# Optimization experiments

Measured on AMD Instinct MI355X. Metric: run time of the kernel, lower is better.

## Reference

```python
import jax, jax.numpy as jnp
import numpy as np

B, D, L = 2, 1024, 4096   # batch, channels (= num_heads), seq len
FS = 4                    # filter_size
DEPTH = 11                # ceil(log2((L-1)/(FS-1)+1))
LN_EPS = 1e-5


def setup_inputs() -> dict:
    key = jax.random.key(0)
    ks = jax.random.split(key, 7)
    return {
        "x": jax.random.normal(ks[0], (B, D, L), jnp.float32),
        "h0": jax.random.normal(ks[1], (D, 1, FS), jnp.float32) * 0.2,
        "h1": jax.random.normal(ks[2], (D, 1, FS), jnp.float32) * 0.2,
        "w_mix": jax.random.normal(ks[3], (D, D), jnp.float32) / np.sqrt(D),
        "b_mix": jnp.zeros((D,), jnp.float32),
        "ln_gamma": jnp.ones((D,), jnp.float32),
        "ln_beta": jnp.zeros((D,), jnp.float32),
    }


def _dw_conv(a, h, dilation):
    # depthwise (groups = D) dilated conv1d, cross-correlation like torch
    return jax.lax.conv_general_dilated(
        a, h, window_strides=(1,), padding='VALID',
        rhs_dilation=(dilation,),
        dimension_numbers=('NCH', 'OIH', 'NCH'),
        feature_group_count=D)


def reference(x, h0, h1, w_mix, b_mix, ln_gamma, ln_beta):
    # --- multires conv tree ---
    a = x
    dilation = 1
    a_list, b_list = [], []
    for _ in range(DEPTH):
        pad = dilation * (FS - 1)
        ap = jnp.pad(a, ((0, 0), (0, 0), (pad, 0)))  # left causal pad
        b = _dw_conv(ap, h1, dilation)
        a = _dw_conv(ap, h0, dilation)
        a_list.append(a)
        b_list.append(b)
        dilation *= 2
    # --- gated combination across scales (deepest level first) ---
    a_rev = a_list[::-1]
    b_rev = b_list[::-1]
    y = jnp.zeros_like(x)
    gated = None
    for i in range(DEPTH):
        if i + 1 < DEPTH:
            gated = jax.nn.sigmoid(a_rev[i]) * b_rev[i + 1]
        # last iteration reuses the previous gated tensor (matches original)
        y = y + gated
    # --- 1x1 channel mix (Dropout1d is identity in eval) + residual ---
    mixed = jnp.einsum('oc,bcl->bol', w_mix, y) + b_mix[None, :, None]
    z = mixed + x
    # --- LayerNorm over channel dim ---
    mu = jnp.mean(z, axis=1, keepdims=True)
    var = jnp.mean(jnp.square(z - mu), axis=1, keepdims=True)
    out = (z - mu) * jax.lax.rsqrt(var + LN_EPS)
    out = out * ln_gamma[None, :, None] + ln_beta[None, :, None]
    return out
```

## Files before the change

### kernel.cpp

```cpp
#include <hip/hip_runtime.h>
#include <hip/hip_bf16.h>

#define NB 2
#define ND 1024
#define NL 4096
#define NFS 4
#define NDEPTH 11
#define LN_EPS 1e-5f

#define BM 128
#define BN 128
#define BK 32
#define NKI (ND / BK)

#define CPAD 1536
#define CBUF (CPAD + NL)

typedef __bf16 bf16x8 __attribute__((ext_vector_type(8)));
typedef float f32x4 __attribute__((ext_vector_type(4)));

__device__ __forceinline__ unsigned short f2bf(float f) {
    __hip_bfloat16 h = __float2bfloat16(f);
    unsigned short u;
    __builtin_memcpy(&u, &h, 2);
    return u;
}

__device__ __forceinline__ float bf2f(unsigned short u) {
    unsigned int ui = (unsigned int)u << 16;
    float f;
    __builtin_memcpy(&f, &ui, 4);
    return f;
}

__device__ __forceinline__ unsigned int pack2bf(float lo, float hi) {
    return (unsigned int)f2bf(lo) | ((unsigned int)f2bf(hi) << 16);
}

__device__ __forceinline__ float sigm(float v) {
    return __builtin_amdgcn_rcpf(1.f + __expf(-v));
}

__device__ __forceinline__ void llds16(const void* g, void* l) {
    __builtin_amdgcn_global_load_lds(
        (const __attribute__((address_space(1))) unsigned int*)g,
        (__attribute__((address_space(3))) unsigned int*)l, 16, 0, 0);
}

__global__ __launch_bounds__(256) void wconv_kernel(const float* __restrict__ w,
                                                    unsigned short* __restrict__ wbf) {
    const int idx8 = (blockIdx.x * 256 + threadIdx.x) * 8;
    const float4 v0 = *reinterpret_cast<const float4*>(w + idx8);
    const float4 v1 = *reinterpret_cast<const float4*>(w + idx8 + 4);
    uint4 o;
    o.x = pack2bf(v0.x, v0.y);
    o.y = pack2bf(v0.z, v0.w);
    o.z = pack2bf(v1.x, v1.y);
    o.w = pack2bf(v1.z, v1.w);
    *reinterpret_cast<uint4*>(wbf + idx8) = o;
}

__global__ __launch_bounds__(256) void conv_cascade_kernel(const float* __restrict__ x,
                                                           const float* __restrict__ h0,
                                                           const float* __restrict__ h1,
                                                           unsigned short* __restrict__ ybf) {
    __shared__ float a_sh[2 * CBUF];
    const int row = blockIdx.x;
    const int d = row & (ND - 1);
    const int t = threadIdx.x;

#pragma unroll
    for (int j = 0; j < 2; ++j)
#pragma unroll
        for (int i = 0; i < CPAD / 256; ++i)
            a_sh[j * CBUF + i * 256 + t] = 0.f;

    const float* xrow = x + (size_t)row * NL;

    float h0c[NFS], h1c[NFS];
#pragma unroll
    for (int k = 0; k < NFS; ++k) {
        h0c[k] = h0[d * NFS + k];
        h1c[k] = h1[d * NFS + k];
    }

    float cur[4][4], yacc[4][4], bprev[4][4];
#pragma unroll
    for (int c = 0; c < 4; ++c) {
        const float4 v = *reinterpret_cast<const float4*>(xrow + c * 1024 + t * 4);
        cur[c][0] = v.x; cur[c][1] = v.y; cur[c][2] = v.z; cur[c][3] = v.w;
        *reinterpret_cast<float4*>(&a_sh[CPAD + c * 1024 + t * 4]) = v;
#pragma unroll
        for (int j = 0; j < 4; ++j) { yacc[c][j] = 0.f; bprev[c][j] = 0.f; }
    }
    __syncthreads();

    int rb = 0, wb = CBUF;

#define CONV_CHUNK(c, A1, A2, A3, SC, WB)                                            \
    {                                                                                \
        float an[4], bn[4];                                                          \
        _Pragma("unroll") for (int j = 0; j < 4; ++j) {                              \
            an[j] = h0c[3] * cur[c][j] + h0c[2] * (A1)[j] + h0c[1] * (A2)[j] +       \
                    h0c[0] * (A3)[j];                                                \
            bn[j] = h1c[3] * cur[c][j] + h1c[2] * (A1)[j] + h1c[1] * (A2)[j] +       \
                    h1c[0] * (A3)[j];                                                \
        }                                                                            \
        if (WB) {                                                                    \
            float4 wv; wv.x = an[0]; wv.y = an[1]; wv.z = an[2]; wv.w = an[3];       \
            *reinterpret_cast<float4*>(&a_sh[wb + CPAD + (c)*1024 + t * 4]) = wv;    \
        }                                                                            \
        if ((SC) > 0.f) {                                                            \
            _Pragma("unroll") for (int j = 0; j < 4; ++j)                            \
                yacc[c][j] += (SC)*sigm(an[j]) * bprev[c][j];                        \
        }                                                                            \
        _Pragma("unroll") for (int j = 0; j < 4; ++j) {                              \
            cur[c][j] = an[j];                                                       \
            bprev[c][j] = bn[j];                                                     \
        }                                                                            \
    }

#pragma unroll
    for (int c = 0; c < 4; ++c) {
        const int A = rb + CPAD + c * 1024 + t * 4;
        const float4 m1 = *reinterpret_cast<const float4*>(&a_sh[A - 4]);
        const float a1[4] = {m1.w, cur[c][0], cur[c][1], cur[c][2]};
        const float a2[4] = {m1.z, m1.w, cur[c][0], cur[c][1]};
        const float a3[4] = {m1.y, m1.z, m1.w, cur[c][0]};
        CONV_CHUNK(c, a1, a2, a3, 0.f, 1)
    }
    { const int tmp = rb; rb = wb; wb = tmp; }
    __syncthreads();

#pragma unroll
    for (int c = 0; c < 4; ++c) {
        const int A = rb + CPAD + c * 1024 + t * 4;
        const float4 m1 = *reinterpret_cast<const float4*>(&a_sh[A - 4]);
        const float4 m2 = *reinterpret_cast<const float4*>(&a_sh[A - 8]);
        const float a1[4] = {m1.z, m1.w, cur[c][0], cur[c][1]};
        const float a2[4] = {m1.x, m1.y, m1.z, m1.w};
        const float a3[4] = {m2.z, m2.w, m1.x, m1.y};
        CONV_CHUNK(c, a1, a2, a3, 2.f, 1)
    }
    { const int tmp = rb; rb = wb; wb = tmp; }
    __syncthreads();

    int dil = 4;
#pragma unroll 1
    for (int lev = 2; lev <= 8; ++lev) {
#pragma unroll
        for (int c = 0; c < 4; ++c) {
            const int A = rb + CPAD + c * 1024 + t * 4;
            const float4 b1 = *reinterpret_cast<const float4*>(&a_sh[A - dil]);
            const float4 b2 = *reinterpret_cast<const float4*>(&a_sh[A - 2 * dil]);
            const float4 b3 = *reinterpret_cast<const float4*>(&a_sh[A - 3 * dil]);
            const float a1[4] = {b1.x, b1.y, b1.z, b1.w};
            const float a2[4] = {b2.x, b2.y, b2.z, b2.w};
            const float a3[4] = {b3.x, b3.y, b3.z, b3.w};
            CONV_CHUNK(c, a1, a2, a3, 1.f, 1)
        }
        { const int tmp = rb; rb = wb; wb = tmp; }
        dil <<= 1;
        __syncthreads();
    }

#pragma unroll
    for (int c = 0; c < 4; ++c) {
        const int A = rb + CPAD + c * 1024 + t * 4;
        const float4 b1 = *reinterpret_cast<const float4*>(&a_sh[A - 512]);
        const float4 b2 = *reinterpret_cast<const float4*>(&a_sh[A - 1024]);
        const float4 b3 = *reinterpret_cast<const float4*>(&a_sh[A - 1536]);
        const float a1[4] = {b1.x, b1.y, b1.z, b1.w};
        const float a2[4] = {b2.x, b2.y, b2.z, b2.w};
        const float a3[4] = {b3.x, b3.y, b3.z, b3.w};
        CONV_CHUNK(c, a1, a2, a3, 1.f, 0)
    }

#pragma unroll
    for (int c = 0; c < 4; ++c) {
#pragma unroll
        for (int j = 0; j < 4; ++j) {
            const float a1 = (c >= 1) ? cur[c - 1][j] : 0.f;
            const float a2 = (c >= 2) ? cur[c - 2][j] : 0.f;
            const float a3 = (c >= 3) ? cur[c - 3][j] : 0.f;
            const float an = h0c[3] * cur[c][j] + h0c[2] * a1 + h0c[1] * a2 + h0c[0] * a3;
            yacc[c][j] += sigm(an) * bprev[c][j];
        }
    }
#undef CONV_CHUNK

#pragma unroll
    for (int c = 0; c < 4; ++c) {
        ushort4 o;
        o.x = f2bf(yacc[c][0]);
        o.y = f2bf(yacc[c][1]);
        o.z = f2bf(yacc[c][2]);
        o.w = f2bf(yacc[c][3]);
        *reinterpret_cast<ushort4*>(ybf + (size_t)row * NL + c * 1024 + t * 4) = o;
    }
}

__global__ __launch_bounds__(256) void transpose_kernel(const unsigned short* __restrict__ ybf,
                                                        unsigned short* __restrict__ yT) {
    __shared__ unsigned short tile[64][66];
    const int l0 = blockIdx.x * 64;
    const int c0 = blockIdx.y * 64;
    const int b = blockIdx.z;
    const int t = threadIdx.x;
    const int li = t & 63, cg = t >> 6;
#pragma unroll
    for (int k = 0; k < 16; ++k) {
        const int ci = cg * 16 + k;
        tile[ci][li] = ybf[(size_t)(b * ND + c0 + ci) * NL + l0 + li];
    }
    __syncthreads();
    const int ci2 = t & 63, lg = t >> 6;
#pragma unroll
    for (int k = 0; k < 16; ++k) {
        const int li2 = lg * 16 + k;
        yT[((size_t)b * NL + l0 + li2) * ND + c0 + ci2] = tile[ci2][li2];
    }
}

__global__ __launch_bounds__(256) void gemm_kernel(const unsigned short* __restrict__ wbf,
                                                   const unsigned short* __restrict__ yT,
                                                   const float* __restrict__ bmix,
                                                   unsigned short* __restrict__ mixed) {
    __shared__ unsigned short As[2][BM][BK];
    __shared__ unsigned short Bs[2][BN][BK];

    const int n0 = blockIdx.x * BN;
    const int m0 = blockIdx.y * BM;
    const int b = blockIdx.z;
    const int t = threadIdx.x;
    const int lane = t & 63, wid = t >> 6;
    const int wr = wid >> 1, wc = wid & 1;
    const int fr = lane & 15;
    const int fk = (lane >> 4) * 8;

    const int srow = wid * 32 + (lane >> 2);
    const int sk = (lane & 3) * 8;
    const unsigned short* Ag = wbf + (size_t)(m0 + srow) * ND + sk;
    const unsigned short* Bg = yT + ((size_t)b * NL + n0 + srow) * ND + sk;
    unsigned short* AsD0[2] = {&As[0][wid * 32][0], &As[1][wid * 32][0]};
    unsigned short* AsD1[2] = {&As[0][wid * 32 + 16][0], &As[1][wid * 32 + 16][0]};
    unsigned short* BsD0[2] = {&Bs[0][wid * 32][0], &Bs[1][wid * 32][0]};
    unsigned short* BsD1[2] = {&Bs[0][wid * 32 + 16][0], &Bs[1][wid * 32 + 16][0]};

    f32x4 acc[4][4];
#pragma unroll
    for (int mi = 0; mi < 4; ++mi)
#pragma unroll
        for (int ni = 0; ni < 4; ++ni)
            acc[mi][ni] = (f32x4){0.f, 0.f, 0.f, 0.f};

    llds16(Ag, AsD0[0]);
    llds16(Ag + 16 * ND, AsD1[0]);
    llds16(Bg, BsD0[0]);
    llds16(Bg + 16 * ND, BsD1[0]);
    asm volatile("s_waitcnt vmcnt(0)" ::: "memory");
    __builtin_amdgcn_s_barrier();

    int cur = 0;
#pragma unroll 1
    for (int ki = 0; ki < NKI; ++ki) {
        if (ki + 1 < NKI) {
            const int kt = (ki + 1) * BK;
            llds16(Ag + kt, AsD0[cur ^ 1]);
            llds16(Ag + kt + 16 * ND, AsD1[cur ^ 1]);
            llds16(Bg + kt, BsD0[cur ^ 1]);
            llds16(Bg + kt + 16 * ND, BsD1[cur ^ 1]);
        }

        bf16x8 af[4], bv[4];
#pragma unroll
        for (int mi = 0; mi < 4; ++mi)
            af[mi] = *reinterpret_cast<const bf16x8*>(&As[cur][wr * 64 + mi * 16 + fr][fk]);
#pragma unroll
        for (int ni = 0; ni < 4; ++ni)
            bv[ni] = *reinterpret_cast<const bf16x8*>(&Bs[cur][wc * 64 + ni * 16 + fr][fk]);
#pragma unroll
        for (int mi = 0; mi < 4; ++mi)
#pragma unroll
            for (int ni = 0; ni < 4; ++ni)
                acc[mi][ni] = __builtin_amdgcn_mfma_f32_16x16x32_bf16(af[mi], bv[ni],
                                                                      acc[mi][ni], 0, 0, 0);

        asm volatile("s_waitcnt vmcnt(0)" ::: "memory");
        __builtin_amdgcn_s_barrier();
        cur ^= 1;
    }

    const size_t bbase = (size_t)b * ND * NL;
#pragma unroll
    for (int mi = 0; mi < 4; ++mi) {
#pragma unroll
        for (int r = 0; r < 4; ++r) {
            const int o = m0 + wr * 64 + mi * 16 + (lane >> 4) * 4 + r;
            const float bm = bmix[o];
            const size_t rowbase = bbase + (size_t)o * NL;
#pragma unroll
            for (int ni = 0; ni < 4; ++ni) {
                const int l = n0 + wc * 64 + ni * 16 + fr;
                mixed[rowbase + l] = f2bf(acc[mi][ni][r] + bm);
            }
        }
    }
}

__global__ __launch_bounds__(512) void ln_kernel(const unsigned short* __restrict__ mixed,
                                                 const float* __restrict__ x,
                                                 const float* __restrict__ gamma,
                                                 const float* __restrict__ beta,
                                                 float* __restrict__ out) {
    const int b = blockIdx.y;
    const int l0 = blockIdx.x * 32;
    const int tl = threadIdx.x & 31, tg = threadIdx.x >> 5;
    const size_t base = (size_t)b * ND * NL + l0 + tl;

    float zv[64];
    float s = 0.f, q = 0.f;
#pragma unroll
    for (int j = 0; j < 64; ++j) {
        const size_t idx = base + (size_t)(tg + j * 16) * NL;
        const float v = bf2f(mixed[idx]) + x[idx];
        zv[j] = v;
        s += v;
        q += v * v;
    }

    __shared__ float sred[16][33], qred[16][33];
    __shared__ float mu_s[32], rs_s[32];
    sred[tg][tl] = s;
    qred[tg][tl] = q;
    __syncthreads();
    if (tg == 0) {
        float S = 0.f, Q = 0.f;
#pragma unroll
        for (int g = 0; g < 16; ++g) {
            S += sred[g][tl];
            Q += qred[g][tl];
        }
        const float mu = S * (1.f / ND);
        const float var = Q * (1.f / ND) - mu * mu;
        mu_s[tl] = mu;
        rs_s[tl] = rsqrtf(var + LN_EPS);
    }
    __syncthreads();
    const float mu = mu_s[tl], rs = rs_s[tl];
#pragma unroll
    for (int j = 0; j < 64; ++j) {
        const int c = tg + j * 16;
        out[base + (size_t)c * NL] = (zv[j] - mu) * rs * gamma[c] + beta[c];
    }
}

extern "C" void kernel_launch(void* const* d_in, const int* in_sizes, int n_in,
                              void* d_out, int out_size, void* d_ws, size_t ws_size,
                              hipStream_t stream) {
    (void)in_sizes; (void)n_in; (void)out_size; (void)ws_size;
    const float* x = (const float*)d_in[0];
    const float* h0 = (const float*)d_in[1];
    const float* h1 = (const float*)d_in[2];
    const float* wmix = (const float*)d_in[3];
    const float* bmix = (const float*)d_in[4];
    const float* gamma = (const float*)d_in[5];
    const float* beta = (const float*)d_in[6];
    float* out = (float*)d_out;

    char* ws = (char*)d_ws;
    unsigned short* ybf = (unsigned short*)(ws);
    unsigned short* yT = (unsigned short*)(ws + (size_t)16 * 1024 * 1024);
    unsigned short* wbf = (unsigned short*)(ws + (size_t)32 * 1024 * 1024);
    unsigned short* mixed = (unsigned short*)(ws + (size_t)34 * 1024 * 1024);

    wconv_kernel<<<dim3(ND * ND / (256 * 8)), 256, 0, stream>>>(wmix, wbf);
    conv_cascade_kernel<<<dim3(NB * ND), 256, 0, stream>>>(x, h0, h1, ybf);
    transpose_kernel<<<dim3(NL / 64, ND / 64, NB), 256, 0, stream>>>(ybf, yT);
    gemm_kernel<<<dim3(NL / BN, ND / BM, NB), 256, 0, stream>>>(wbf, yT, bmix, mixed);
    ln_kernel<<<dim3(NL / 32, NB), 512, 0, stream>>>(mixed, x, gamma, beta, out);
}
```

Baseline: 105.8 us.

## Single-buffer conv cascade with 512 threads; triple-buffer GEMM LDS pipeline

The conv cascade kernel now runs 512 threads per row, each handling two 4-wide chunks. It uses a single LDS buffer with a larger causal pad instead of ping-pong buffers, and an extra barrier separates the reads from the writes. Levels 9 and 10 move into the shared-memory loop and the final level reads from LDS. The GEMM switches from double to triple buffering with two stages prefetched ahead and a partial vmcnt wait, so global loads overlap more MFMA work. This adds barriers in the conv kernel and more LDS use in the GEMM, which may lower occupancy.

```diff
diff --git a/kernel.cpp b/kernel.cpp
--- a/kernel.cpp
+++ b/kernel.cpp
@@ -12,8 +12,9 @@
 #define BN 128
 #define BK 32
 #define NKI (ND / BK)
-
-#define CPAD 1536
+#define ASZ (BM * BK)
+
+#define CPAD 3072
 #define CBUF (CPAD + NL)
 
 typedef __bf16 bf16x8 __attribute__((ext_vector_type(8)));
@@ -60,20 +61,17 @@
     *reinterpret_cast<uint4*>(wbf + idx8) = o;
 }
 
-__global__ __launch_bounds__(256) void conv_cascade_kernel(const float* __restrict__ x,
-                                                           const float* __restrict__ h0,
-                                                           const float* __restrict__ h1,
-                                                           unsigned short* __restrict__ ybf) {
-    __shared__ float a_sh[2 * CBUF];
+__global__ __launch_bounds__(512, 8) void conv_cascade_kernel(const float* __restrict__ x,
+                                                              const float* __restrict__ h0,
+                                                              const float* __restrict__ h1,
+                                                              unsigned short* __restrict__ ybf) {
+    __shared__ float a_sh[CBUF];
     const int row = blockIdx.x;
     const int d = row & (ND - 1);
     const int t = threadIdx.x;
 
 #pragma unroll
-    for (int j = 0; j < 2; ++j)
-#pragma unroll
-        for (int i = 0; i < CPAD / 256; ++i)
-            a_sh[j * CBUF + i * 256 + t] = 0.f;
+    for (int i = 0; i < CPAD / 512; ++i) a_sh[i * 512 + t] = 0.f;
 
     const float* xrow = x + (size_t)row * NL;
 
@@ -84,32 +82,28 @@
         h1c[k] = h1[d * NFS + k];
     }
 
-    float cur[4][4], yacc[4][4], bprev[4][4];
-#pragma unroll
-    for (int c = 0; c < 4; ++c) {
-        const float4 v = *reinterpret_cast<const float4*>(xrow + c * 1024 + t * 4);
+    float cur[2][4], yacc[2][4], bprev[2][4];
+#pragma unroll
+    for (int c = 0; c < 2; ++c) {
+        const float4 v = *reinterpret_cast<const float4*>(xrow + c * 2048 + t * 4);
         cur[c][0] = v.x; cur[c][1] = v.y; cur[c][2] = v.z; cur[c][3] = v.w;
-        *reinterpret_cast<float4*>(&a_sh[CPAD + c * 1024 + t * 4]) = v;
+        *reinterpret_cast<float4*>(&a_sh[CPAD + c * 2048 + t * 4]) = v;
 #pragma unroll
         for (int j = 0; j < 4; ++j) { yacc[c][j] = 0.f; bprev[c][j] = 0.f; }
     }
     __syncthreads();
 
-    int rb = 0, wb = CBUF;
-
-#define CONV_CHUNK(c, A1, A2, A3, SC, WB)                                            \
+#define CONV_MATH(c, A1, A2, A3, an, bn)                                             \
+    _Pragma("unroll") for (int j = 0; j < 4; ++j) {                                  \
+        an[j] = h0c[3] * cur[c][j] + h0c[2] * (A1)[j] + h0c[1] * (A2)[j] +           \
+                h0c[0] * (A3)[j];                                                    \
+        bn[j] = h1c[3] * cur[c][j] + h1c[2] * (A1)[j] + h1c[1] * (A2)[j] +           \
+                h1c[0] * (A3)[j];                                                    \
+    }
+#define CONV_FIN(c, an, bn, SC)                                                      \
     {                                                                                \
-        float an[4], bn[4];                                                          \
-        _Pragma("unroll") for (int j = 0; j < 4; ++j) {                              \
-            an[j] = h0c[3] * cur[c][j] + h0c[2] * (A1)[j] + h0c[1] * (A2)[j] +       \
-                    h0c[0] * (A3)[j];                                                \
-            bn[j] = h1c[3] * cur[c][j] + h1c[2] * (A1)[j] + h1c[1] * (A2)[j] +       \
-                    h1c[0] * (A3)[j];                                                \
-        }                                                                            \
-        if (WB) {                                                                    \
-            float4 wv; wv.x = an[0]; wv.y = an[1]; wv.z = an[2]; wv.w = an[3];       \
-            *reinterpret_cast<float4*>(&a_sh[wb + CPAD + (c)*1024 + t * 4]) = wv;    \
-        }                                                                            \
+        float4 wv; wv.x = an[0]; wv.y = an[1]; wv.z = an[2]; wv.w = an[3];           \
+        *reinterpret_cast<float4*>(&a_sh[CPAD + (c)*2048 + t * 4]) = wv;             \
         if ((SC) > 0.f) {                                                            \
             _Pragma("unroll") for (int j = 0; j < 4; ++j)                            \
                 yacc[c][j] += (SC)*sigm(an[j]) * bprev[c][j];                        \
@@ -120,83 +114,111 @@
         }                                                                            \
     }
 
-#pragma unroll
-    for (int c = 0; c < 4; ++c) {
-        const int A = rb + CPAD + c * 1024 + t * 4;
-        const float4 m1 = *reinterpret_cast<const float4*>(&a_sh[A - 4]);
-        const float a1[4] = {m1.w, cur[c][0], cur[c][1], cur[c][2]};
-        const float a2[4] = {m1.z, m1.w, cur[c][0], cur[c][1]};
-        const float a3[4] = {m1.y, m1.z, m1.w, cur[c][0]};
-        CONV_CHUNK(c, a1, a2, a3, 0.f, 1)
-    }
-    { const int tmp = rb; rb = wb; wb = tmp; }
-    __syncthreads();
-
-#pragma unroll
-    for (int c = 0; c < 4; ++c) {
-        const int A = rb + CPAD + c * 1024 + t * 4;
-        const float4 m1 = *reinterpret_cast<const float4*>(&a_sh[A - 4]);
-        const float4 m2 = *reinterpret_cast<const float4*>(&a_sh[A - 8]);
-        const float a1[4] = {m1.z, m1.w, cur[c][0], cur[c][1]};
-        const float a2[4] = {m1.x, m1.y, m1.z, m1.w};
-        const float a3[4] = {m2.z, m2.w, m1.x, m1.y};
-        CONV_CHUNK(c, a1, a2, a3, 2.f, 1)
-    }
-    { const int tmp = rb; rb = wb; wb = tmp; }
-    __syncthreads();
+    float an0[4], bn0[4], an1[4], bn1[4];
+
+    {
+        {
+            const int A = CPAD + 0 * 2048 + t * 4;
+            const float4 m1 = *reinterpret_cast<const float4*>(&a_sh[A - 4]);
+            const float a1[4] = {m1.w, cur[0][0], cur[0][1], cur[0][2]};
+            const float a2[4] = {m1.z, m1.w, cur[0][0], cur[0][1]};
+            const float a3[4] = {m1.y, m1.z, m1.w, cur[0][0]};
+            CONV_MATH(0, a1, a2, a3, an0, bn0)
+        }
+        {
+            const int A = CPAD + 1 * 2048 + t * 4;
+            const float4 m1 = *reinterpret_cast<const float4*>(&a_sh[A - 4]);
+            const float a1[4] = {m1.w, cur[1][0], cur[1][1], cur[1][2]};
+            const float a2[4] = {m1.z, m1.w, cur[1][0], cur[1][1]};
+            const float a3[4] = {m1.y, m1.z, m1.w, cur[1][0]};
+            CONV_MATH(1, a1, a2, a3, an1, bn1)
+        }
+        __syncthreads();
+        CONV_FIN(0, an0, bn0, 0.f)
+        CONV_FIN(1, an1, bn1, 0.f)
+        __syncthreads();
+    }
+
+    {
+        {
+            const int A = CPAD + 0 * 2048 + t * 4;
+            const float4 m1 = *reinterpret_cast<const float4*>(&a_sh[A - 4]);
+            const float4 m2 = *reinterpret_cast<const float4*>(&a_sh[A - 8]);
+            const float a1[4] = {m1.z, m1.w, cur[0][0], cur[0][1]};
+            const float a2[4] = {m1.x, m1.y, m1.z, m1.w};
+            const float a3[4] = {m2.z, m2.w, m1.x, m1.y};
+            CONV_MATH(0, a1, a2, a3, an0, bn0)
+        }
+        {
+            const int A = CPAD + 1 * 2048 + t * 4;
+            const float4 m1 = *reinterpret_cast<const float4*>(&a_sh[A - 4]);
+            const float4 m2 = *reinterpret_cast<const float4*>(&a_sh[A - 8]);
+            const float a1[4] = {m1.z, m1.w, cur[1][0], cur[1][1]};
+            const float a2[4] = {m1.x, m1.y, m1.z, m1.w};
+            const float a3[4] = {m2.z, m2.w, m1.x, m1.y};
+            CONV_MATH(1, a1, a2, a3, an1, bn1)
+        }
+        __syncthreads();
+        CONV_FIN(0, an0, bn0, 2.f)
+        CONV_FIN(1, an1, bn1, 2.f)
+        __syncthreads();
+    }
 
     int dil = 4;
 #pragma unroll 1
-    for (int lev = 2; lev <= 8; ++lev) {
-#pragma unroll
-        for (int c = 0; c < 4; ++c) {
-            const int A = rb + CPAD + c * 1024 + t * 4;
+    for (int lev = 2; lev <= 9; ++lev) {
+        {
+            const int A = CPAD + 0 * 2048 + t * 4;
             const float4 b1 = *reinterpret_cast<const float4*>(&a_sh[A - dil]);
             const float4 b2 = *reinterpret_cast<const float4*>(&a_sh[A - 2 * dil]);
             const float4 b3 = *reinterpret_cast<const float4*>(&a_sh[A - 3 * dil]);
             const float a1[4] = {b1.x, b1.y, b1.z, b1.w};
             const float a2[4] = {b2.x, b2.y, b2.z, b2.w};
             const float a3[4] = {b3.x, b3.y, b3.z, b3.w};
-            CONV_CHUNK(c, a1, a2, a3, 1.f, 1)
-        }
-        { const int tmp = rb; rb = wb; wb = tmp; }
+            CONV_MATH(0, a1, a2, a3, an0, bn0)
+        }
+        {
+            const int A = CPAD + 1 * 2048 + t * 4;
+            const float4 b1 = *reinterpret_cast<const float4*>(&a_sh[A - dil]);
+            const float4 b2 = *reinterpret_cast<const float4*>(&a_sh[A - 2 * dil]);
+            const float4 b3 = *reinterpret_cast<const float4*>(&a_sh[A - 3 * dil]);
+            const float a1[4] = {b1.x, b1.y, b1.z, b1.w};
+            const float a2[4] = {b2.x, b2.y, b2.z, b2.w};
+            const float a3[4] = {b3.x, b3.y, b3.z, b3.w};
+            CONV_MATH(1, a1, a2, a3, an1, bn1)
+        }
+        __syncthreads();
+        CONV_FIN(0, an0, bn0, 1.f)
+        CONV_FIN(1, an1, bn1, 1.f)
         dil <<= 1;
         __syncthreads();
     }
 
 #pragma unroll
-    for (int c = 0; c < 4; ++c) {
-        const int A = rb + CPAD + c * 1024 + t * 4;
-        const float4 b1 = *reinterpret_cast<const float4*>(&a_sh[A - 512]);
-        const float4 b2 = *reinterpret_cast<const float4*>(&a_sh[A - 1024]);
-        const float4 b3 = *reinterpret_cast<const float4*>(&a_sh[A - 1536]);
-        const float a1[4] = {b1.x, b1.y, b1.z, b1.w};
-        const float a2[4] = {b2.x, b2.y, b2.z, b2.w};
-        const float a3[4] = {b3.x, b3.y, b3.z, b3.w};
-        CONV_CHUNK(c, a1, a2, a3, 1.f, 0)
-    }
-
-#pragma unroll
-    for (int c = 0; c < 4; ++c) {
+    for (int c = 0; c < 2; ++c) {
+        const int A = CPAD + c * 2048 + t * 4;
+        const float4 b1 = *reinterpret_cast<const float4*>(&a_sh[A - 1024]);
+        const float4 b3 = *reinterpret_cast<const float4*>(&a_sh[A - 3072]);
 #pragma unroll
         for (int j = 0; j < 4; ++j) {
-            const float a1 = (c >= 1) ? cur[c - 1][j] : 0.f;
-            const float a2 = (c >= 2) ? cur[c - 2][j] : 0.f;
-            const float a3 = (c >= 3) ? cur[c - 3][j] : 0.f;
+            const float a1 = (&b1.x)[j];
+            const float a2 = (c == 1) ? cur[0][j] : 0.f;
+            const float a3 = (&b3.x)[j];
             const float an = h0c[3] * cur[c][j] + h0c[2] * a1 + h0c[1] * a2 + h0c[0] * a3;
             yacc[c][j] += sigm(an) * bprev[c][j];
         }
     }
-#undef CONV_CHUNK
-
-#pragma unroll
-    for (int c = 0; c < 4; ++c) {
+#undef CONV_MATH
+#undef CONV_FIN
+
+#pragma unroll
+    for (int c = 0; c < 2; ++c) {
         ushort4 o;
         o.x = f2bf(yacc[c][0]);
         o.y = f2bf(yacc[c][1]);
         o.z = f2bf(yacc[c][2]);
         o.w = f2bf(yacc[c][3]);
-        *reinterpret_cast<ushort4*>(ybf + (size_t)row * NL + c * 1024 + t * 4) = o;
+        *reinterpret_cast<ushort4*>(ybf + (size_t)row * NL + c * 2048 + t * 4) = o;
     }
 }
 
@@ -226,8 +248,8 @@
                                                    const unsigned short* __restrict__ yT,
                                                    const float* __restrict__ bmix,
                                                    unsigned short* __restrict__ mixed) {
-    __shared__ unsigned short As[2][BM][BK];
-    __shared__ unsigned short Bs[2][BN][BK];
+    __shared__ unsigned short As[3][BM][BK];
+    __shared__ unsigned short Bs[3][BN][BK];
 
     const int n0 = blockIdx.x * BN;
     const int m0 = blockIdx.y * BM;
@@ -242,10 +264,16 @@
     const int sk = (lane & 3) * 8;
     const unsigned short* Ag = wbf + (size_t)(m0 + srow) * ND + sk;
     const unsigned short* Bg = yT + ((size_t)b * NL + n0 + srow) * ND + sk;
-    unsigned short* AsD0[2] = {&As[0][wid * 32][0], &As[1][wid * 32][0]};
-    unsigned short* AsD1[2] = {&As[0][wid * 32 + 16][0], &As[1][wid * 32 + 16][0]};
-    unsigned short* BsD0[2] = {&Bs[0][wid * 32][0], &Bs[1][wid * 32][0]};
-    unsigned short* BsD1[2] = {&Bs[0][wid * 32 + 16][0], &Bs[1][wid * 32 + 16][0]};
+    unsigned short* A0 = &As[0][0][0];
+    unsigned short* B0 = &Bs[0][0][0];
+    unsigned short* AsW = A0 + wid * 32 * BK;
+    unsigned short* BsW = B0 + wid * 32 * BK;
+
+#define STAGE(bo, kt)                           \
+    llds16(Ag + (kt), AsW + (bo));              \
+    llds16(Ag + (kt) + 16 * ND, AsW + (bo) + 16 * BK); \
+    llds16(Bg + (kt), BsW + (bo));              \
+    llds16(Bg + (kt) + 16 * ND, BsW + (bo) + 16 * BK);
 
     f32x4 acc[4][4];
 #pragma unroll
@@ -254,42 +282,45 @@
         for (int ni = 0; ni < 4; ++ni)
             acc[mi][ni] = (f32x4){0.f, 0.f, 0.f, 0.f};
 
-    llds16(Ag, AsD0[0]);
-    llds16(Ag + 16 * ND, AsD1[0]);
-    llds16(Bg, BsD0[0]);
-    llds16(Bg + 16 * ND, BsD1[0]);
-    asm volatile("s_waitcnt vmcnt(0)" ::: "memory");
-    __builtin_amdgcn_s_barrier();
-
-    int cur = 0;
+    STAGE(0, 0)
+    STAGE(ASZ, BK)
+
+    int bc = 0;
+    int bs = 2;
 #pragma unroll 1
     for (int ki = 0; ki < NKI; ++ki) {
         if (ki + 1 < NKI) {
-            const int kt = (ki + 1) * BK;
-            llds16(Ag + kt, AsD0[cur ^ 1]);
-            llds16(Ag + kt + 16 * ND, AsD1[cur ^ 1]);
-            llds16(Bg + kt, BsD0[cur ^ 1]);
-            llds16(Bg + kt + 16 * ND, BsD1[cur ^ 1]);
-        }
-
+            asm volatile("s_waitcnt vmcnt(4)" ::: "memory");
+        } else {
+            asm volatile("s_waitcnt vmcnt(0)" ::: "memory");
+        }
+        __builtin_amdgcn_s_barrier();
+        __builtin_amdgcn_sched_barrier(0);
+
+        if (ki + 2 < NKI) {
+            const int bo = bs * ASZ;
+            const int kt = (ki + 2) * BK;
+            STAGE(bo, kt)
+        }
+
+        const int bco = bc * ASZ;
         bf16x8 af[4], bv[4];
 #pragma unroll
         for (int mi = 0; mi < 4; ++mi)
-            af[mi] = *reinterpret_cast<const bf16x8*>(&As[cur][wr * 64 + mi * 16 + fr][fk]);
+            af[mi] = *reinterpret_cast<const bf16x8*>(A0 + bco + (wr * 64 + mi * 16 + fr) * BK + fk);
 #pragma unroll
         for (int ni = 0; ni < 4; ++ni)
-            bv[ni] = *reinterpret_cast<const bf16x8*>(&Bs[cur][wc * 64 + ni * 16 + fr][fk]);
+            bv[ni] = *reinterpret_cast<const bf16x8*>(B0 + bco + (wc * 64 + ni * 16 + fr) * BK + fk);
 #pragma unroll
         for (int mi = 0; mi < 4; ++mi)
 #pragma unroll
             for (int ni = 0; ni < 4; ++ni)
                 acc[mi][ni] = __builtin_amdgcn_mfma_f32_16x16x32_bf16(af[mi], bv[ni],
                                                                       acc[mi][ni], 0, 0, 0);
-
-        asm volatile("s_waitcnt vmcnt(0)" ::: "memory");
-        __builtin_amdgcn_s_barrier();
-        cur ^= 1;
-    }
+        bc = (bc == 2) ? 0 : bc + 1;
+        bs = (bs == 2) ? 0 : bs + 1;
+    }
+#undef STAGE
 
     const size_t bbase = (size_t)b * ND * NL;
 #pragma unroll
@@ -375,7 +406,7 @@
     unsigned short* mixed = (unsigned short*)(ws + (size_t)34 * 1024 * 1024);
 
     wconv_kernel<<<dim3(ND * ND / (256 * 8)), 256, 0, stream>>>(wmix, wbf);
-    conv_cascade_kernel<<<dim3(NB * ND), 256, 0, stream>>>(x, h0, h1, ybf);
+    conv_cascade_kernel<<<dim3(NB * ND), 512, 0, stream>>>(x, h0, h1, ybf);
     transpose_kernel<<<dim3(NL / 64, ND / 64, NB), 256, 0, stream>>>(ybf, yT);
     gemm_kernel<<<dim3(NL / BN, ND / BM, NB), 256, 0, stream>>>(wbf, yT, bmix, mixed);
     ln_kernel<<<dim3(NL / 32, NB), 512, 0, stream>>>(mixed, x, gamma, beta, out);
```

After: 104.2 us. No clear change (-1.6%).
